# Performance work log

Hardware: AMD Instinct MI355X
Metric: run time of the kernel (lower is better)

Reference implementation:

```python
import jax, jax.numpy as jnp
import numpy as np

L, LM, B, D, H, DFF = 1024, 1024, 2, 512, 8, 2048
N = 16              # mamba d_state
DI = 2 * D          # mamba d_inner (expand=2)
DCONV = 4
DTR = (D + 15) // 16  # dt_rank = 32
EPS = 1e-5


def _rmsnorm(x, w):
    return x * w / jnp.sqrt(jnp.mean(x * x, -1, keepdims=True) + EPS)


def _layernorm(x, w, b):
    m = jnp.mean(x, -1, keepdims=True)
    v = jnp.mean((x - m) ** 2, -1, keepdims=True)
    return (x - m) / jnp.sqrt(v + EPS) * w + b


def _mha(q, k, v, in_w, in_b, out_w, out_b):
    # q: [Lq,B,D]; k,v: [Lk,B,D]
    Lq, Bb, Dd = q.shape
    Lk = k.shape[0]
    dh = Dd // H
    qp = (q @ in_w[:Dd].T + in_b[:Dd]).reshape(Lq, Bb, H, dh).transpose(1, 2, 0, 3)
    kp = (k @ in_w[Dd:2 * Dd].T + in_b[Dd:2 * Dd]).reshape(Lk, Bb, H, dh).transpose(1, 2, 0, 3)
    vp = (v @ in_w[2 * Dd:].T + in_b[2 * Dd:]).reshape(Lk, Bb, H, dh).transpose(1, 2, 0, 3)
    s = jnp.einsum('bhqd,bhkd->bhqk', qp, kp) * (dh ** -0.5)
    a = jax.nn.softmax(s, axis=-1)
    o = jnp.einsum('bhqk,bhkd->bhqd', a, vp).transpose(2, 0, 1, 3).reshape(Lq, Bb, Dd)
    return o @ out_w.T + out_b, jnp.mean(a, axis=1)  # attn averaged over heads


def _mamba(x, in_w, in_b, conv_w, conv_b, xproj_w, dt_w, dt_b, Alog, Dp, out_w, out_b):
    # x: [B,L,D] -> [B,L,D] selective state-space scan (mamba.py MambaBlock)
    xz = x @ in_w.T + in_b
    xm, z = xz[..., :DI], xz[..., DI:]
    # causal depthwise conv over time (pad left d_conv-1, truncate to L)
    xc = jax.lax.conv_general_dilated(
        xm.transpose(0, 2, 1), conv_w[:, None, :], (1,), [(DCONV - 1, 0)],
        feature_group_count=DI, dimension_numbers=('NCH', 'OIH', 'NCH'))
    xm = jax.nn.silu((xc + conv_b[None, :, None]).transpose(0, 2, 1))  # [B,L,DI]
    dbc = xm @ xproj_w.T
    dt, Bs, Cs = dbc[..., :DTR], dbc[..., DTR:DTR + N], dbc[..., DTR + N:]
    delta = jax.nn.softplus(dt @ dt_w.T + dt_b)           # [B,L,DI]
    A = -jnp.exp(Alog)                                    # [DI,N]
    dA = jnp.exp(delta[..., None] * A)                    # [B,L,DI,N]
    dBx = delta[..., None] * Bs[:, :, None, :] * xm[..., None]

    def step(h, ab):
        a, b = ab
        h = a * h + b
        return h, h

    _, hs = jax.lax.scan(step, jnp.zeros((x.shape[0], DI, N), x.dtype),
                         (dA.transpose(1, 0, 2, 3), dBx.transpose(1, 0, 2, 3)))
    y = jnp.einsum('blin,bln->bli', hs.transpose(1, 0, 2, 3), Cs)
    y = (y + Dp * xm) * jax.nn.silu(z)
    return y @ out_w.T + out_b


def _bimamba(x, ln1_w, ln1_b, ln2_w, ln2_b, f1_w, f1_b, f2_w, f2_b, mp):
    xn = _layernorm(x, ln1_w, ln1_b)
    mf = _mamba(xn, *mp)
    mb = jnp.flip(_mamba(jnp.flip(xn, 1), *mp), 1)
    m = _layernorm(mf + mb, ln2_w, ln2_b)
    ff = jax.nn.gelu(m @ f1_w.T + f1_b, approximate=False) @ f2_w.T + f2_b
    return ff + x


def _forward(tgt, memory,
             sa_in_w, sa_in_b, sa_out_w, sa_out_b,
             ca_in_w, ca_in_b, ca_out_w, ca_out_b,
             n1_w, n2_w, n3_w, n4_w,
             lin1_w, lin1_b, lin2_w, lin2_b,
             ln1_w, ln1_b, ln2_w, ln2_b,
             bff1_w, bff1_b, bff2_w, bff2_b,
             m_in_w, m_in_b, m_conv_w, m_conv_b, m_xproj_w,
             m_dt_w, m_dt_b, m_Alog, m_D, m_out_w, m_out_b):
    t2, _ = _mha(tgt, tgt, tgt, sa_in_w, sa_in_b, sa_out_w, sa_out_b)
    tgt = _rmsnorm(tgt + t2, n1_w)
    t2, attn = _mha(tgt, memory, memory, ca_in_w, ca_in_b, ca_out_w, ca_out_b)
    tgt = _rmsnorm(tgt + t2, n2_w)
    x = tgt.transpose(1, 0, 2)  # l b d -> b l d
    mp = (m_in_w, m_in_b, m_conv_w, m_conv_b, m_xproj_w, m_dt_w, m_dt_b, m_Alog, m_D, m_out_w, m_out_b)
    x = x + _bimamba(x, ln1_w, ln1_b, ln2_w, ln2_b, bff1_w, bff1_b, bff2_w, bff2_b, mp)
    tgt = x.transpose(1, 0, 2)
    tgt = _rmsnorm(tgt, n3_w)
    t2 = jax.nn.relu(tgt @ lin1_w.T + lin1_b) @ lin2_w.T + lin2_b
    tgt = _rmsnorm(tgt + t2, n4_w)
    return tgt, attn


def setup_inputs() -> dict:
    key = jax.random.key(0)
    ks = jax.random.split(key, 24)
    g = lambda i, shape, s=0.02: jax.random.normal(ks[i], shape, dtype=jnp.float32) * s
    inp = {
        'tgt': jax.random.normal(ks[0], (L, B, D), dtype=jnp.float32),
        'memory': jax.random.normal(ks[1], (LM, B, D), dtype=jnp.float32),
        'sa_in_w': g(2, (3 * D, D)), 'sa_in_b': jnp.zeros((3 * D,)),
        'sa_out_w': g(3, (D, D)), 'sa_out_b': jnp.zeros((D,)),
        'ca_in_w': g(4, (3 * D, D)), 'ca_in_b': jnp.zeros((3 * D,)),
        'ca_out_w': g(5, (D, D)), 'ca_out_b': jnp.zeros((D,)),
        'n1_w': jnp.ones((D,)), 'n2_w': jnp.ones((D,)),
        'n3_w': jnp.ones((D,)), 'n4_w': jnp.ones((D,)),
        'lin1_w': g(6, (DFF, D)), 'lin1_b': jnp.zeros((DFF,)),
        'lin2_w': g(7, (D, DFF)), 'lin2_b': jnp.zeros((D,)),
        'ln1_w': jnp.ones((D,)), 'ln1_b': jnp.zeros((D,)),
        'ln2_w': jnp.ones((D,)), 'ln2_b': jnp.zeros((D,)),
        'bff1_w': g(8, (4 * D, D)), 'bff1_b': jnp.zeros((4 * D,)),
        'bff2_w': g(9, (D, 4 * D)), 'bff2_b': jnp.zeros((D,)),
        'm_in_w': g(10, (2 * DI, D)), 'm_in_b': jnp.zeros((2 * DI,)),
        'm_conv_w': g(11, (DI, DCONV), 0.1), 'm_conv_b': jnp.zeros((DI,)),
        'm_xproj_w': g(12, (DTR + 2 * N, DI)),
        'm_dt_w': g(13, (DI, DTR), 0.1), 'm_dt_b': g(14, (DI,), 0.01),
        'm_Alog': jnp.log(jnp.tile(jnp.arange(1, N + 1, dtype=jnp.float32), (DI, 1))),
        'm_D': jnp.ones((DI,)),
        'm_out_w': g(15, (D, DI)), 'm_out_b': jnp.zeros((D,)),
    }
    return inp


def reference(tgt, memory,
              sa_in_w, sa_in_b, sa_out_w, sa_out_b,
              ca_in_w, ca_in_b, ca_out_w, ca_out_b,
              n1_w, n2_w, n3_w, n4_w,
              lin1_w, lin1_b, lin2_w, lin2_b,
              ln1_w, ln1_b, ln2_w, ln2_b,
              bff1_w, bff1_b, bff2_w, bff2_b,
              m_in_w, m_in_b, m_conv_w, m_conv_b, m_xproj_w,
              m_dt_w, m_dt_b, m_Alog, m_D, m_out_w, m_out_b):
    return _forward(tgt, memory,
                    sa_in_w, sa_in_b, sa_out_w, sa_out_b,
                    ca_in_w, ca_in_b, ca_out_w, ca_out_b,
                    n1_w, n2_w, n3_w, n4_w,
                    lin1_w, lin1_b, lin2_w, lin2_b,
                    ln1_w, ln1_b, ln2_w, ln2_b,
                    bff1_w, bff1_b, bff2_w, bff2_b,
                    m_in_w, m_in_b, m_conv_w, m_conv_b, m_xproj_w,
                    m_dt_w, m_dt_b, m_Alog, m_D, m_out_w, m_out_b)
```

## Files before the change

kernel.cpp:

```cpp
#include <hip/hip_runtime.h>
#include <hip/hip_bf16.h>
#include <math.h>

#define L_SEQ 1024
#define BB 2
#define DD 512
#define HH 8
#define DFFN 2048
#define NSTATE 16
#define DI 1024
#define EPSF 1e-5f

typedef __hip_bfloat16 bf16;
typedef __attribute__((ext_vector_type(8))) short short8v;
typedef __attribute__((ext_vector_type(4))) short short4v;
typedef __attribute__((ext_vector_type(4))) float float4v;

__device__ __forceinline__ float bf2f(bf16 v){ return __bfloat162float(v); }
__device__ __forceinline__ bf16 f2bf(float v){ return __float2bfloat16(v); }
__device__ __forceinline__ short f2bfs(float v){
  bf16 t = __float2bfloat16(v);
  short s; __builtin_memcpy(&s, &t, 2);
  return s;
}

__global__ void k_detect(const unsigned int* __restrict__ w, int* __restrict__ flag){
  __shared__ int cnt;
  if (threadIdx.x==0) cnt = 0;
  __syncthreads();
  unsigned int x = w[threadIdx.x];
  unsigned int low = x & 0xffffu;
  int e = (int)((low >> 7) & 0xffu);
  int vote = (low==0u) || (e >= 110 && e <= 140);
  atomicAdd(&cnt, vote);
  __syncthreads();
  if (threadIdx.x==0) flag[0] = (cnt >= 128) ? 1 : 0;
}

struct CvtTabF { const void* src[25]; unsigned int off[26]; };
struct CvtTabW { const void* src[12]; unsigned int off[13]; };

__global__ __launch_bounds__(256) void k_cvt_f32(CvtTabF t, float* __restrict__ dst,
                                                 const int* __restrict__ flag, int total){
  const int isbf = flag[0];
  for (int g = blockIdx.x*256 + threadIdx.x; g < total; g += gridDim.x*256){
    int k = 0;
    while (t.off[k+1] <= (unsigned int)g) ++k;
    int e = g - (int)t.off[k];
    dst[g] = isbf ? bf2f(((const bf16*)t.src[k])[e]) : ((const float*)t.src[k])[e];
  }
}

__global__ __launch_bounds__(256) void k_cvt_b16(CvtTabW t, bf16* __restrict__ dst,
                                                 const int* __restrict__ flag, int total){
  const int isbf = flag[0];
  for (int g = blockIdx.x*256 + threadIdx.x; g < total; g += gridDim.x*256){
    int k = 0;
    while (t.off[k+1] <= (unsigned int)g) ++k;
    int e = g - (int)t.off[k];
    if (isbf) dst[g] = ((const bf16*)t.src[k])[e];
    else      dst[g] = f2bf(((const float*)t.src[k])[e]);
  }
}

__global__ __launch_bounds__(256) void k_mfma_gemm(
    const void* __restrict__ Ab, int cA, long long sAb, long long sAh, long long sAm,
    const void* __restrict__ Bb, long long sBb, long long sBh, long long sBrow, int cB,
    void* __restrict__ Cb, int outBf, long long sCb, long long sCh, long long sCm,
    const float* __restrict__ bias, float scale, int act, int K, int H)
{
  __shared__ short As[64*40];
  __shared__ short Bs[64*40];
  const int tid = threadIdx.x;
  int bx = blockIdx.x, by = blockIdx.y;
  if (gridDim.z == 1 && (gridDim.y & 7) == 0){
    int gx = gridDim.x;
    int lin = by*gx + bx;
    int xcd = lin & 7, i = lin >> 3;
    by = xcd*(gridDim.y >> 3) + i / gx;
    bx = i % gx;
  }
  const int z = blockIdx.z; const int zb = z / H; const int zh = z % H;
  const int col0 = bx << 6, m0 = by << 6;
  const float* Af = (const float*)Ab;
  const bf16*  Aw = (const bf16*)Ab;
  const long long aoff = zb*sAb + zh*sAh;
  const float* Bf = (const float*)Bb;
  const bf16* Bw = (const bf16*)Bb;
  const long long boff = zb*sBb + zh*sBh;
  float4v acc[4];
  #pragma unroll
  for (int i=0;i<4;++i) acc[i] = (float4v)(0.f);
  const int lane = tid & 63, w = tid >> 6;
  const int lr = lane & 15, quad = lane >> 4;

  for (int k0 = 0; k0 < K; k0 += 32){
    if (cA == 1){
      int row = tid >> 2, k8 = (tid & 3) << 3;
      short8v v = *(const short8v*)&Aw[aoff + (long long)(m0+row)*sAm + k0 + k8];
      *(short8v*)&As[row*40 + k8] = v;
    } else {
      #pragma unroll
      for (int i=0;i<2;++i){
        int g = tid + i*256;
        int row = g >> 3, k4 = (g & 7) << 2;
        float4 v = *(const float4*)&Af[aoff + (long long)(m0+row)*sAm + k0 + k4];
        short4v s4; s4.x=f2bfs(v.x); s4.y=f2bfs(v.y); s4.z=f2bfs(v.z); s4.w=f2bfs(v.w);
        *(short4v*)&As[row*40 + k4] = s4;
      }
    }
    if (cB == 2){
      int row = tid >> 2, k8 = (tid & 3) << 3;
      short8v v = *(const short8v*)&Bw[boff + (long long)(col0+row)*sBrow + k0 + k8];
      *(short8v*)&Bs[row*40 + k8] = v;
    } else {
      #pragma unroll
      for (int i=0;i<2;++i){
        int g = tid + i*256;
        int row = g >> 3, k4 = (g & 7) << 2;
        float4 v = *(const float4*)&Bf[boff + (long long)(col0+row)*sBrow + k0 + k4];
        short4v s4; s4.x=f2bfs(v.x); s4.y=f2bfs(v.y); s4.z=f2bfs(v.z); s4.w=f2bfs(v.w);
        *(short4v*)&Bs[row*40 + k4] = s4;
      }
    }
    __syncthreads();
    short8v a = *(short8v*)&As[(w*16 + lr)*40 + quad*8];
    #pragma unroll
    for (int cb=0; cb<4; ++cb){
      short8v bfr = *(short8v*)&Bs[(cb*16 + lr)*40 + quad*8];
      acc[cb] = __builtin_amdgcn_mfma_f32_16x16x32_bf16(a, bfr, acc[cb], 0, 0, 0);
    }
    __syncthreads();
  }
  #pragma unroll
  for (int cb=0; cb<4; ++cb){
    #pragma unroll
    for (int r=0;r<4;++r){
      int m = m0 + w*16 + quad*4 + r;
      int n = col0 + cb*16 + lr;
      float v = acc[cb][r] * scale;
      if (bias) v += bias[n];
      if (act==1) v = fmaxf(v,0.f);
      else if (act==2) v = 0.5f*v*(1.f + erff(v*0.70710678118654752f));
      else if (act==3) v = fmaxf(v,0.f) + log1pf(__expf(-fabsf(v)));
      if (outBf) ((bf16*)Cb)[zb*sCb + zh*sCh + (long long)m*sCm + n] = f2bf(v);
      else       ((float*)Cb)[zb*sCb + zh*sCh + (long long)m*sCm + n] = v;
    }
  }
}

__global__ __launch_bounds__(256) void k_gemm_sk(
    const void* __restrict__ Ab, int cA, long long sAz, long long sAm,
    const bf16* __restrict__ Bw, long long sBrow,
    float* __restrict__ Cb, long long sCz, long long sCm,
    const float* __restrict__ bias, int K, int KS)
{
  __shared__ short As[64*40];
  __shared__ short Bs[64*40];
  const int tid = threadIdx.x;
  int bx, by, bz;
  {
    int gx = gridDim.x, gy = gridDim.y, gz = gridDim.z;
    int lin = ((int)blockIdx.z*gy + blockIdx.y)*gx + blockIdx.x;
    int xcd = lin & 7, i = lin >> 3;
    bx = i % gx; int rest = i / gx;
    int pair = xcd * ((gy*gz) >> 3) + rest;
    by = pair % gy; bz = pair / gy;
  }
  const int zb = bz / KS, kc = bz % KS;
  const int Kc = K / KS;
  const int col0 = bx << 6, m0 = by << 6;
  const float* Af = (const float*)Ab;
  const bf16*  Aw = (const bf16*)Ab;
  const long long aoff = (long long)zb*sAz;
  float4v acc[4];
  #pragma unroll
  for (int i=0;i<4;++i) acc[i] = (float4v)(0.f);
  const int lane = tid & 63, w = tid >> 6;
  const int lr = lane & 15, quad = lane >> 4;

  const int kbeg = kc*Kc;
  for (int k0 = kbeg; k0 < kbeg + Kc; k0 += 32){
    if (cA == 1){
      int row = tid >> 2, k8 = (tid & 3) << 3;
      *(short8v*)&As[row*40 + k8] =
        *(const short8v*)&Aw[aoff + (long long)(m0+row)*sAm + k0 + k8];
    } else {
      #pragma unroll
      for (int i=0;i<2;++i){
        int g = tid + i*256;
        int row = g >> 3, k4 = (g & 7) << 2;
        float4 v = *(const float4*)&Af[aoff + (long long)(m0+row)*sAm + k0 + k4];
        short4v s4; s4.x=f2bfs(v.x); s4.y=f2bfs(v.y); s4.z=f2bfs(v.z); s4.w=f2bfs(v.w);
        *(short4v*)&As[row*40 + k4] = s4;
      }
    }
    {
      int row = tid >> 2, k8 = (tid & 3) << 3;
      *(short8v*)&Bs[row*40 + k8] =
        *(const short8v*)&Bw[(long long)(col0+row)*sBrow + k0 + k8];
    }
    __syncthreads();
    short8v a = *(short8v*)&As[(w*16 + lr)*40 + quad*8];
    #pragma unroll
    for (int cb=0; cb<4; ++cb){
      short8v bfr = *(short8v*)&Bs[(cb*16 + lr)*40 + quad*8];
      acc[cb] = __builtin_amdgcn_mfma_f32_16x16x32_bf16(a, bfr, acc[cb], 0, 0, 0);
    }
    __syncthreads();
  }
  #pragma unroll
  for (int cb=0; cb<4; ++cb){
    #pragma unroll
    for (int r=0;r<4;++r){
      int m = m0 + w*16 + quad*4 + r;
      int n = col0 + cb*16 + lr;
      float v = acc[cb][r];
      if (kc == 0 && bias) v += bias[n];
      atomicAdd(&Cb[(long long)zb*sCz + (long long)m*sCm + n], v);
    }
  }
}

__global__ __launch_bounds__(256) void k_flash2(
    const bf16* __restrict__ Qb, int ldq, int qoff,
    const bf16* __restrict__ Kb, int ldk, int koff,
    const bf16* __restrict__ Vb, int ldv, int voff,
    float* __restrict__ Opart, float* __restrict__ Ml, float scale)
{
  __shared__ short Qs[64*40];
  __shared__ short Ks[64*40];
  __shared__ short Vs[64*40];
  __shared__ short Ps[64*40];
  const int tid = threadIdx.x;
  const int q0 = blockIdx.x << 6;
  const int z = blockIdx.y; const int b = z >> 3; const int hoff = (z & 7) << 6;
  const int kc = blockIdx.z;
  const int lane = tid & 63, w = tid >> 6;
  const int lr = lane & 15, quad = lane >> 4;

  #pragma unroll
  for (int i=0;i<2;++i){
    int idx = tid + i*256;
    int row = idx >> 3, d8 = (idx & 7) << 3;
    *(short8v*)&Qs[row*40 + d8] =
      *(const short8v*)&Qb[(size_t)((q0+row)*BB + b)*ldq + qoff + hoff + d8];
  }

  float m_r[4], l_r[4];
  #pragma unroll
  for (int r=0;r<4;++r){ m_r[r] = -1e30f; l_r[r] = 0.f; }
  float4v acc_o[4];
  #pragma unroll
  for (int cb=0;cb<4;++cb) acc_o[cb] = (float4v)(0.f);

  short8v kr[2], vr[2];
  #pragma unroll
  for (int i=0;i<2;++i){
    int idx = tid + i*256;
    int row = kc*256 + (idx >> 3); int d8 = (idx & 7) << 3;
    kr[i] = *(const short8v*)&Kb[(size_t)(row*BB + b)*ldk + koff + hoff + d8];
    vr[i] = *(const short8v*)&Vb[(size_t)(row*BB + b)*ldv + voff + hoff + d8];
  }

  for (int kt=0; kt<4; ++kt){
    __syncthreads();
    #pragma unroll
    for (int i=0;i<2;++i){
      int idx = tid + i*256;
      int row = idx >> 3, d8 = (idx & 7) << 3;
      *(short8v*)&Ks[row*40 + d8] = kr[i];
      int sc = row ^ d8;
      #pragma unroll
      for (int j=0;j<8;++j) Vs[(d8+j)*40 + sc] = vr[i][j];
    }
    if (kt < 3){
      #pragma unroll
      for (int i=0;i<2;++i){
        int idx = tid + i*256;
        int row = kc*256 + (kt+1)*64 + (idx >> 3); int d8 = (idx & 7) << 3;
        kr[i] = *(const short8v*)&Kb[(size_t)(row*BB + b)*ldk + koff + hoff + d8];
        vr[i] = *(const short8v*)&Vb[(size_t)(row*BB + b)*ldv + voff + hoff + d8];
      }
    }
    __syncthreads();
    short8v a0 = *(short8v*)&Qs[(w*16+lr)*40 + quad*8];
    short8v a1 = *(short8v*)&Qs[(w*16+lr)*40 + quad*8 + 32];
    float4v s[4];
    #pragma unroll
    for (int cb=0;cb<4;++cb){
      short8v b0 = *(short8v*)&Ks[(cb*16+lr)*40 + quad*8];
      short8v b1 = *(short8v*)&Ks[(cb*16+lr)*40 + quad*8 + 32];
      float4v t = __builtin_amdgcn_mfma_f32_16x16x32_bf16(a0, b0, (float4v)(0.f), 0,0,0);
      s[cb] = __builtin_amdgcn_mfma_f32_16x16x32_bf16(a1, b1, t, 0,0,0);
    }
    #pragma unroll
    for (int cb=0;cb<4;++cb)
      #pragma unroll
      for (int r=0;r<4;++r) s[cb][r] *= scale;
    float al[4];
    #pragma unroll
    for (int r=0;r<4;++r){
      float mx = fmaxf(fmaxf(s[0][r],s[1][r]),fmaxf(s[2][r],s[3][r]));
      #pragma unroll
      for (int ofs=1; ofs<16; ofs<<=1) mx = fmaxf(mx, __shfl_xor(mx, ofs));
      float mnew = fmaxf(m_r[r], mx);
      al[r] = __expf(m_r[r] - mnew);
      float sum = 0.f;
      #pragma unroll
      for (int cb=0;cb<4;++cb){
        float p = __expf(s[cb][r] - mnew);
        s[cb][r] = p;
        sum += p;
      }
      #pragma unroll
      for (int ofs=1; ofs<16; ofs<<=1) sum += __shfl_xor(sum, ofs);
      l_r[r] = l_r[r]*al[r] + sum;
      m_r[r] = mnew;
    }
    #pragma unroll
    for (int cb=0;cb<4;++cb)
      #pragma unroll
      for (int r=0;r<4;++r){
        acc_o[cb][r] *= al[r];
        Ps[(w*16 + quad*4 + r)*40 + cb*16 + lr] = f2bfs(s[cb][r]);
      }
    __syncthreads();
    short8v p0 = *(short8v*)&Ps[(w*16+lr)*40 + quad*8];
    short8v p1 = *(short8v*)&Ps[(w*16+lr)*40 + quad*8 + 32];
    #pragma unroll
    for (int cb=0;cb<4;++cb){
      int dcol = cb*16 + lr;
      int sw = (dcol >> 3) & 7;
      short8v v0 = *(short8v*)&Vs[dcol*40 + ((quad ^ sw) << 3)];
      short8v v1 = *(short8v*)&Vs[dcol*40 + (((quad+4) ^ sw) << 3)];
      acc_o[cb] = __builtin_amdgcn_mfma_f32_16x16x32_bf16(p0, v0, acc_o[cb], 0,0,0);
      acc_o[cb] = __builtin_amdgcn_mfma_f32_16x16x32_bf16(p1, v1, acc_o[cb], 0,0,0);
    }
  }
  #pragma unroll
  for (int r=0;r<4;++r){
    int row = q0 + w*16 + quad*4 + r;
    size_t obase = ((size_t)(kc*16 + z)*1024 + row)*64;
    #pragma unroll
    for (int cb=0;cb<4;++cb)
      Opart[obase + cb*16 + lr] = acc_o[cb][r];
    if (lr == 0){
      size_t mi = ((size_t)kc*16384 + z*1024 + row)*2;
      Ml[mi] = m_r[r]; Ml[mi+1] = l_r[r];
    }
  }
}

__global__ __launch_bounds__(256) void k_fcomb(const float* __restrict__ Opart, const float* __restrict__ Ml,
                                               bf16* __restrict__ O, float* __restrict__ Mfin)
{
  int gid = blockIdx.x*256 + threadIdx.x;
  int row = gid >> 6, d = gid & 63;
  int z = row >> 10, q = row & 1023;
  float m[4], l[4];
  #pragma unroll
  for (int kc=0;kc<4;++kc){
    size_t mi = ((size_t)kc*16384 + row)*2;
    m[kc] = Ml[mi]; l[kc] = Ml[mi+1];
  }
  float ms = fmaxf(fmaxf(m[0],m[1]),fmaxf(m[2],m[3]));
  float c[4]; float ls = 0.f;
  #pragma unroll
  for (int kc=0;kc<4;++kc){ c[kc] = __expf(m[kc]-ms); ls += l[kc]*c[kc]; }
  float o = 0.f;
  #pragma unroll
  for (int kc=0;kc<4;++kc) o += Opart[((size_t)kc*16384 + row)*64 + d] * c[kc];
  o /= ls;
  int b = z >> 3, hoff = (z & 7) << 6;
  O[((size_t)q*BB + b)*512 + hoff + d] = f2bf(o);
  if (d == 0){ Mfin[(size_t)row*2] = ms; Mfin[(size_t)row*2+1] = ls; }
}

__global__ __launch_bounds__(256) void k_pmean(
    const bf16* __restrict__ Qb, int ldq,
    const bf16* __restrict__ Kb, int ldk,
    const float* __restrict__ Mfin, void* __restrict__ out,
    const int* __restrict__ flag, float scale)
{
  __shared__ short Qs[64*40];
  __shared__ short Ks[64*40];
  const int tid = threadIdx.x;
  const int k0 = blockIdx.x << 6, q0 = blockIdx.y << 6;
  const int b = blockIdx.z;
  const int lane = tid & 63, w = tid >> 6;
  const int lr = lane & 15, quad = lane >> 4;
  float acc[4][4];
  #pragma unroll
  for (int cb=0;cb<4;++cb)
    #pragma unroll
    for (int r=0;r<4;++r) acc[cb][r] = 0.f;

  for (int h=0; h<8; ++h){
    int z = b*8 + h, hoff = h << 6;
    __syncthreads();
    #pragma unroll
    for (int i=0;i<2;++i){
      int idx = tid + i*256;
      int row = idx >> 3, d8 = (idx & 7) << 3;
      *(short8v*)&Qs[row*40 + d8] = *(const short8v*)&Qb[((size_t)(q0+row)*BB + b)*ldq + hoff + d8];
      *(short8v*)&Ks[row*40 + d8] = *(const short8v*)&Kb[((size_t)(k0+row)*BB + b)*ldk + hoff + d8];
    }
    __syncthreads();
    float mm[4], li[4];
    #pragma unroll
    for (int r=0;r<4;++r){
      int qrow = q0 + w*16 + quad*4 + r;
      size_t mi = ((size_t)z*1024 + qrow)*2;
      mm[r] = Mfin[mi]; li[r] = 1.f/Mfin[mi+1];
    }
    short8v a0 = *(short8v*)&Qs[(w*16+lr)*40 + quad*8];
    short8v a1 = *(short8v*)&Qs[(w*16+lr)*40 + quad*8 + 32];
    #pragma unroll
    for (int cb=0;cb<4;++cb){
      short8v b0 = *(short8v*)&Ks[(cb*16+lr)*40 + quad*8];
      short8v b1 = *(short8v*)&Ks[(cb*16+lr)*40 + quad*8 + 32];
      float4v t = __builtin_amdgcn_mfma_f32_16x16x32_bf16(a0, b0, (float4v)(0.f), 0,0,0);
      t = __builtin_amdgcn_mfma_f32_16x16x32_bf16(a1, b1, t, 0,0,0);
      #pragma unroll
      for (int r=0;r<4;++r)
        acc[cb][r] += __expf(t[r]*scale - mm[r]) * li[r];
    }
  }
  #pragma unroll
  for (int cb=0;cb<4;++cb)
    #pragma unroll
    for (int r=0;r<4;++r){
      int q = q0 + w*16 + quad*4 + r;
      int k = k0 + cb*16 + lr;
      float v = acc[cb][r] * 0.125f;
      size_t o = (size_t)(1u<<20) + ((size_t)b<<20) + (size_t)q*1024 + k;
      if (flag[0]) ((bf16*)out)[o] = f2bf(v);
      else         ((float*)out)[o] = v;
    }
}

__global__ __launch_bounds__(256) void k_add_rmsnorm(float* __restrict__ x, const float* __restrict__ t2, const float* __restrict__ w){
  int row = blockIdx.x; size_t base = (size_t)row*DD;
  int tid = threadIdx.x;
  float v0 = x[base+tid] + t2[base+tid];
  float v1 = x[base+tid+256] + t2[base+tid+256];
  __shared__ float red[256];
  red[tid] = v0*v0 + v1*v1; __syncthreads();
  for (int s=128;s>0;s>>=1){ if(tid<s) red[tid]+=red[tid+s]; __syncthreads(); }
  float rms = rsqrtf(red[0]*(1.f/DD) + EPSF);
  x[base+tid]     = v0 * w[tid]     * rms;
  x[base+tid+256] = v1 * w[tid+256] * rms;
}

__global__ __launch_bounds__(256) void k_add_rmsnorm_out(const float* __restrict__ x, const float* __restrict__ t2,
                                                         const float* __restrict__ w, void* __restrict__ out,
                                                         const int* __restrict__ flag){
  int row = blockIdx.x; size_t base = (size_t)row*DD;
  int tid = threadIdx.x;
  float v0 = x[base+tid] + t2[base+tid];
  float v1 = x[base+tid+256] + t2[base+tid+256];
  __shared__ float red[256];
  red[tid] = v0*v0 + v1*v1; __syncthreads();
  for (int s=128;s>0;s>>=1){ if(tid<s) red[tid]+=red[tid+s]; __syncthreads(); }
  float rms = rsqrtf(red[0]*(1.f/DD) + EPSF);
  float o0 = v0 * w[tid]     * rms;
  float o1 = v1 * w[tid+256] * rms;
  if (flag[0]){ ((bf16*)out)[base+tid] = f2bf(o0); ((bf16*)out)[base+tid+256] = f2bf(o1); }
  else        { ((float*)out)[base+tid] = o0;      ((float*)out)[base+tid+256] = o1; }
}

__global__ __launch_bounds__(256) void k_trans_layernorm(const float* __restrict__ tgt, const float* __restrict__ w, const float* __restrict__ bias, bf16* __restrict__ xn){
  int r = blockIdx.x;
  int b = r >> 10, l = r & 1023;
  size_t src = ((size_t)l*BB + b)*DD;
  int tid = threadIdx.x;
  float v0 = tgt[src+tid], v1 = tgt[src+tid+256];
  __shared__ float red[256];
  red[tid] = v0 + v1; __syncthreads();
  for (int s=128;s>0;s>>=1){ if(tid<s) red[tid]+=red[tid+s]; __syncthreads(); }
  float mean = red[0]*(1.f/DD);
  __syncthreads();
  red[tid] = v0*v0 + v1*v1; __syncthreads();
  for (int s=128;s>0;s>>=1){ if(tid<s) red[tid]+=red[tid+s]; __syncthreads(); }
  float var = red[0]*(1.f/DD) - mean*mean;
  float rstd = rsqrtf(var + EPSF);
  size_t dst = (size_t)r*DD;
  xn[dst+tid]     = f2bf((v0-mean)*rstd*w[tid]     + bias[tid]);
  xn[dst+tid+256] = f2bf((v1-mean)*rstd*w[tid+256] + bias[tid+256]);
}

__global__ __launch_bounds__(256) void k_combine_ln(const float* __restrict__ yf, const float* __restrict__ yb, const float* __restrict__ w, const float* __restrict__ bias, bf16* __restrict__ mo){
  int r = blockIdx.x; int b = r>>10, l = r&1023;
  size_t rf = (size_t)r*DD;
  size_t rb = ((size_t)(b<<10) + (1023 - l))*DD;
  int tid = threadIdx.x;
  float v0 = yf[rf+tid]     + yb[rb+tid];
  float v1 = yf[rf+tid+256] + yb[rb+tid+256];
  __shared__ float red[256];
  red[tid] = v0 + v1; __syncthreads();
  for (int s=128;s>0;s>>=1){ if(tid<s) red[tid]+=red[tid+s]; __syncthreads(); }
  float mean = red[0]*(1.f/DD);
  __syncthreads();
  red[tid] = v0*v0 + v1*v1; __syncthreads();
  for (int s=128;s>0;s>>=1){ if(tid<s) red[tid]+=red[tid+s]; __syncthreads(); }
  float var = red[0]*(1.f/DD) - mean*mean;
  float rstd = rsqrtf(var + EPSF);
  mo[rf+tid]     = f2bf((v0-mean)*rstd*w[tid]     + bias[tid]);
  mo[rf+tid+256] = f2bf((v1-mean)*rstd*w[tid+256] + bias[tid+256]);
}

__global__ __launch_bounds__(256) void k_bimamba_final(float* __restrict__ tgt, const float* __restrict__ ffo, const float* __restrict__ w){
  int r = blockIdx.x; int b = r>>10, l = r&1023;
  size_t t = ((size_t)l*BB + b)*DD;
  size_t f = (size_t)r*DD;
  int tid = threadIdx.x;
  float v0 = 2.f*tgt[t+tid]     + ffo[f+tid];
  float v1 = 2.f*tgt[t+tid+256] + ffo[f+tid+256];
  __shared__ float red[256];
  red[tid] = v0*v0 + v1*v1; __syncthreads();
  for (int s=128;s>0;s>>=1){ if(tid<s) red[tid]+=red[tid+s]; __syncthreads(); }
  float rms = rsqrtf(red[0]*(1.f/DD) + EPSF);
  tgt[t+tid]     = v0 * w[tid]     * rms;
  tgt[t+tid+256] = v1 * w[tid+256] * rms;
}

__global__ __launch_bounds__(256) void k_conv_silu(const float* __restrict__ xz, const float* __restrict__ cw, const float* __restrict__ cb, float* __restrict__ xmc){
  int rev = blockIdx.y;
  int idx = blockIdx.x*256 + threadIdx.x;
  int c = idx & 1023;
  int l = (idx >> 10) & 1023;
  int b = idx >> 20;
  float acc = cb[c];
  float w4[4];
  #pragma unroll
  for (int j=0;j<4;++j) w4[j] = cw[(c<<2)+j];
  #pragma unroll
  for (int j=0;j<4;++j){
    int t = l - 3 + j;
    if (t >= 0){
      int src = rev ? (1023 - t) : t;
      acc = fmaf(w4[j], xz[((size_t)(b<<10) + src)*2048 + c], acc);
    }
  }
  xmc[(size_t)rev*(2u<<20) + idx] = acc / (1.f + __expf(-acc));
}

__global__ __launch_bounds__(256) void k_scan1(
    const float* __restrict__ delta_f, const float* __restrict__ delta_b,
    const float* __restrict__ xmc_f,  const float* __restrict__ xmc_b,
    const float* __restrict__ dbc_f,  const float* __restrict__ dbc_b,
    const float* __restrict__ Alog,
    float* __restrict__ hend, float* __restrict__ Sdl)
{
  int ch = blockIdx.x*256 + threadIdx.x;
  int c = blockIdx.y;
  int dir = ch >> 11, b = (ch >> 10) & 1, d = ch & 1023;
  const float* delta = dir ? delta_b : delta_f;
  const float* xmc   = dir ? xmc_b   : xmc_f;
  const float* dbc   = dir ? dbc_b   : dbc_f;
  float Av[NSTATE];
  #pragma unroll
  for (int n=0;n<NSTATE;++n) Av[n] = -__expf(Alog[d*NSTATE+n]);
  float h[NSTATE];
  #pragma unroll
  for (int n=0;n<NSTATE;++n) h[n]=0.f;
  float S = 0.f;
  int r0 = b*1024 + c*32;
  for (int t=0;t<32;++t){
    int r = r0 + t;
    float dl = delta[((size_t)r<<10) + d];
    float x  = xmc[((size_t)r<<10) + d];
    const float4* bp = (const float4*)(dbc + (size_t)r*64 + 32);
    float Bv[NSTATE];
    ((float4*)Bv)[0]=bp[0]; ((float4*)Bv)[1]=bp[1]; ((float4*)Bv)[2]=bp[2]; ((float4*)Bv)[3]=bp[3];
    S += dl;
    float dx = dl*x;
    #pragma unroll
    for (int n=0;n<NSTATE;++n){
      float dA = __expf(dl*Av[n]);
      h[n] = fmaf(dA, h[n], dx*Bv[n]);
    }
  }
  size_t base = ((size_t)c*4096 + ch)*16;
  #pragma unroll
  for (int n=0;n<NSTATE;++n) hend[base+n] = h[n];
  Sdl[c*4096 + ch] = S;
}

__global__ __launch_bounds__(256) void k_scan_carry(const float* __restrict__ Alog,
                                                    float* __restrict__ hh, const float* __restrict__ Sdl)
{
  int g = blockIdx.x*256 + threadIdx.x;
  int ch = g >> 4, n = g & 15;
  int d = ch & 1023;
  float Av = -__expf(Alog[d*16+n]);
  float h = 0.f;
  for (int c=0;c<32;++c){
    size_t base = ((size_t)c*4096 + ch)*16 + n;
    float he = hh[base];
    hh[base] = h;
    h = fmaf(__expf(Av*Sdl[c*4096+ch]), h, he);
  }
}

__global__ __launch_bounds__(256) void k_scan2(
    const float* __restrict__ delta_f, const float* __restrict__ delta_b,
    const float* __restrict__ xmc_f,  const float* __restrict__ xmc_b,
    const float* __restrict__ dbc_f,  const float* __restrict__ dbc_b,
    const float* __restrict__ Alog,   const float* __restrict__ hin,
    const float* __restrict__ xz,     const float* __restrict__ Dp,
    bf16* __restrict__ yo)
{
  int ch = blockIdx.x*256 + threadIdx.x;
  int c = blockIdx.y;
  int dir = ch >> 11, b = (ch >> 10) & 1, d = ch & 1023;
  const float* delta = dir ? delta_b : delta_f;
  const float* xmc   = dir ? xmc_b   : xmc_f;
  const float* dbc   = dir ? dbc_b   : dbc_f;
  float Av[NSTATE];
  #pragma unroll
  for (int n=0;n<NSTATE;++n) Av[n] = -__expf(Alog[d*NSTATE+n]);
  float h[NSTATE];
  size_t cbase = ((size_t)c*4096 + ch)*16;
  #pragma unroll
  for (int n=0;n<NSTATE;++n) h[n] = hin[cbase+n];
  float Dd = Dp[d];
  int r0 = b*1024 + c*32;
  for (int t=0;t<32;++t){
    int r = r0 + t;
    int lidx = c*32 + t;
    float dl = delta[((size_t)r<<10) + d];
    float x  = xmc[((size_t)r<<10) + d];
    const float4* bp = (const float4*)(dbc + (size_t)r*64 + 32);
    float Bv[NSTATE], Cv[NSTATE];
    ((float4*)Bv)[0]=bp[0]; ((float4*)Bv)[1]=bp[1]; ((float4*)Bv)[2]=bp[2]; ((float4*)Bv)[3]=bp[3];
    ((float4*)Cv)[0]=bp[4]; ((float4*)Cv)[1]=bp[5]; ((float4*)Cv)[2]=bp[6]; ((float4*)Cv)[3]=bp[7];
    float dx = dl*x;
    float acc = 0.f;
    #pragma unroll
    for (int n=0;n<NSTATE;++n){
      float dA = __expf(dl*Av[n]);
      h[n] = fmaf(dA, h[n], dx*Bv[n]);
      acc = fmaf(h[n], Cv[n], acc);
    }
    int src = dir ? (1023 - lidx) : lidx;
    float zz = xz[((size_t)(b<<10) + src)*2048 + 1024 + d];
    float sg = zz / (1.f + __expf(-zz));
    yo[(size_t)dir*(2u<<20) + ((size_t)r<<10) + d] = f2bf((acc + Dd*x) * sg);
  }
}

extern "C" void kernel_launch(void* const* d_in, const int* in_sizes, int n_in,
                              void* d_out, int out_size, void* d_ws, size_t ws_size,
                              hipStream_t stream)
{
  if (n_in < 37) return;
  static const unsigned int SZ[37] = {
    1048576,1048576,786432,1536,262144,512,786432,1536,262144,512,
    512,512,512,512,1048576,2048,1048576,512,512,512,
    512,512,1048576,2048,1048576,512,1048576,2048,4096,1024,
    65536,32768,1024,16384,1024,524288,512
  };
  static const unsigned char ISW[37] = {
    0,0,1,0,1,0,1,0,1,0, 0,0,0,0,1,0,1,0,0,0,
    0,0,1,0,1,0,1,0,0,0, 1,1,0,0,0,1,0
  };
  const long long MF = 1u<<20;
  if (ws_size < (size_t)(32*MF)*sizeof(float)) return;

  float* ws = (float*)d_ws;
  float* inF = ws;
  bf16*  inB = (bf16*)(ws + 3*MF);
  float* t2    = ws + 7*MF;
  float* mbuf  = ws + 8*MF;
  float* proj  = ws + 9*MF;
  float* big   = ws + 12*MF;
  float* ff1   = ws + 28*MF;
  float* hend  = ws + 30*MF;

  CvtTabF tf; CvtTabW tb;
  unsigned int fOff[37], bOff[37];
  {
    int nf=0, nb=0; unsigned int of=0, ob=0;
    for (int i=0;i<37;++i){
      if (ISW[i]){ tb.src[nb]=d_in[i]; tb.off[nb]=ob; bOff[i]=ob; ob+=SZ[i]; ++nb; }
      else       { tf.src[nf]=d_in[i]; tf.off[nf]=of; fOff[i]=of; of+=SZ[i]; ++nf; }
    }
    tf.off[25]=of; tb.off[12]=ob;
    int* flag = (int*)(ws + 3*MF - 16);

    #define PF(i) (inF + fOff[i])
    #define PW(i) (inB + bOff[i])

    float* tgt_f = PF(0);
    float* mem_f = PF(1);
    bf16* qkvB   = (bf16*)proj;
    bf16* qB     = (bf16*)proj;
    bf16* kvB    = (bf16*)(proj + 1*MF);
    bf16* attnoB = (bf16*)mbuf;
    bf16* xnB    = (bf16*)t2;
    float* Opart   = big;
    float* Ml      = big + 4*MF;
    float* Mfin    = big + 4*MF + 131072;
    float* xz      = big;
    float* xmc_f   = big + 4*MF;
    float* xmc_b   = xmc_f + 2*MF;
    float* delta_f = big + 8*MF;
    float* delta_b = big + 10*MF;
    float* dbc_f   = proj;
    float* dbc_b   = proj + 131072;
    float* Sdl     = proj + 262144;
    float* yproj_f = proj + 1*MF;
    float* yproj_b = proj + 2*MF;
    float* ffo     = mem_f;
    bf16*  ybf     = (bf16*)ff1;
    bf16*  ff1B    = (bf16*)ff1;
    bf16*  mbufB   = (bf16*)mbuf;

    k_detect<<<1,256,0,stream>>>((const unsigned int*)d_in[0], flag);
    k_cvt_f32<<<2048,256,0,stream>>>(tf, inF, flag, (int)of);
    k_cvt_b16<<<4096,256,0,stream>>>(tb, inB, flag, (int)ob);

    k_mfma_gemm<<<dim3(24,32,1),256,0,stream>>>(tgt_f,0,0,0,512, PW(2),0,0,512,2, qkvB,1,0,0,1536, PF(3),1.f,0,512,1);
    k_flash2<<<dim3(16,16,4),256,0,stream>>>(qkvB,1536,0, qkvB,1536,512, qkvB,1536,1024, Opart, Ml, 0.125f);
    k_fcomb<<<4096,256,0,stream>>>(Opart, Ml, attnoB, Mfin);
    hipMemsetAsync(t2, 0, (size_t)MF*4, stream);
    k_gemm_sk<<<dim3(8,32,2),256,0,stream>>>(attnoB,1,0,512, PW(4),512, t2,0,512, PF(5), 512, 2);
    k_add_rmsnorm<<<2048,256,0,stream>>>(tgt_f, t2, PF(10));

    k_mfma_gemm<<<dim3(8,32,1),256,0,stream>>>(tgt_f,0,0,0,512, PW(6),0,0,512,2, qB,1,0,0,512, PF(7),1.f,0,512,1);
    k_mfma_gemm<<<dim3(16,32,1),256,0,stream>>>(mem_f,0,0,0,512, PW(6)+(size_t)512*512,0,0,512,2, kvB,1,0,0,1024, PF(7)+512,1.f,0,512,1);
    k_flash2<<<dim3(16,16,4),256,0,stream>>>(qB,512,0, kvB,1024,0, kvB,1024,512, Opart, Ml, 0.125f);
    k_fcomb<<<4096,256,0,stream>>>(Opart, Ml, attnoB, Mfin);
    k_pmean<<<dim3(16,16,2),256,0,stream>>>(qB,512, kvB,1024, Mfin, d_out, flag, 0.125f);
    hipMemsetAsync(t2, 0, (size_t)MF*4, stream);
    k_gemm_sk<<<dim3(8,32,2),256,0,stream>>>(attnoB,1,0,512, PW(8),512, t2,0,512, PF(9), 512, 2);
    k_add_rmsnorm<<<2048,256,0,stream>>>(tgt_f, t2, PF(11));

    k_trans_layernorm<<<2048,256,0,stream>>>(tgt_f, PF(18), PF(19), xnB);
    k_mfma_gemm<<<dim3(32,32,1),256,0,stream>>>(xnB,1,0,0,512, PW(26),0,0,512,2, xz,0,0,0,2048, PF(27),1.f,0,512,1);
    k_conv_silu<<<dim3(8192,2),256,0,stream>>>(xz, PF(28), PF(29), xmc_f);
    hipMemsetAsync(dbc_f, 0, (size_t)262144*4, stream);
    k_gemm_sk<<<dim3(1,32,8),256,0,stream>>>(xmc_f,0,2*MF,1024, PW(30),1024, dbc_f,131072,64, nullptr, 1024, 4);
    k_mfma_gemm<<<dim3(16,32,2),256,0,stream>>>(dbc_f,0,131072,0,64, PW(31),0,0,32,2, delta_f,0,2*MF,0,1024, PF(32),1.f,3,32,1);
    k_scan1<<<dim3(16,32),256,0,stream>>>(delta_f,delta_b,xmc_f,xmc_b,dbc_f,dbc_b, PF(33), hend, Sdl);
    k_scan_carry<<<256,256,0,stream>>>(PF(33), hend, Sdl);
    k_scan2<<<dim3(16,32),256,0,stream>>>(delta_f,delta_b,xmc_f,xmc_b,dbc_f,dbc_b, PF(33), hend, xz, PF(34), ybf);
    hipMemsetAsync(yproj_f, 0, (size_t)2*MF*4, stream);
    k_gemm_sk<<<dim3(8,32,4),256,0,stream>>>(ybf,1,2*MF,1024, PW(35),1024, yproj_f,1*MF,512, PF(36), 1024, 2);
    k_combine_ln<<<2048,256,0,stream>>>(yproj_f, yproj_b, PF(20), PF(21), mbufB);
    k_mfma_gemm<<<dim3(32,32,1),256,0,stream>>>(mbufB,1,0,0,512, PW(22),0,0,512,2, ff1B,1,0,0,2048, PF(23),1.f,2,512,1);
    hipMemsetAsync(ffo, 0, (size_t)MF*4, stream);
    k_gemm_sk<<<dim3(8,32,4),256,0,stream>>>(ff1B,1,0,2048, PW(24),2048, ffo,0,512, PF(25), 2048, 4);
    k_bimamba_final<<<2048,256,0,stream>>>(tgt_f, ffo, PF(12));

    k_mfma_gemm<<<dim3(32,32,1),256,0,stream>>>(tgt_f,0,0,0,512, PW(14),0,0,512,2, ff1B,1,0,0,2048, PF(15),1.f,1,512,1);
    hipMemsetAsync(t2, 0, (size_t)MF*4, stream);
    k_gemm_sk<<<dim3(8,32,4),256,0,stream>>>(ff1B,1,0,2048, PW(16),2048, t2,0,512, PF(17), 2048, 4);
    k_add_rmsnorm_out<<<2048,256,0,stream>>>(tgt_f, t2, PF(13), d_out, flag);
    #undef PF
    #undef PW
  }
}
```

Measured before the change: 625.7 us.

## Split flash and scan into more chunks, store mamba intermediates in bf16, use power-table decay

Flash attention now splits the key range into 8 chunks instead of 4, and the combine kernel merges 8 partial results. The selective scan uses 64 time chunks of 16 instead of 32 of 32, and the scratch buffers are moved to make room for this. The conv/silu output and delta are stored as bf16 to halve their memory traffic. When A matches -(n+1), which holds for the test initialisation, the 16 decay exponentials are replaced by powers of a single exp(-delta). A runtime check falls back to the exact path otherwise, and the bf16 storage lowers precision.

```diff
diff --git a/kernel.cpp b/kernel.cpp
--- a/kernel.cpp
+++ b/kernel.cpp
@@ -22,6 +22,14 @@
   bf16 t = __float2bfloat16(v);
   short s; __builtin_memcpy(&s, &t, 2);
   return s;
+}
+
+__device__ __forceinline__ void powtab(float q1, float* dA){
+  float q2=q1*q1, q4=q2*q2, q8=q4*q4;
+  dA[0]=q1;       dA[1]=q2;       dA[2]=q2*q1;     dA[3]=q4;
+  dA[4]=q4*q1;    dA[5]=q4*q2;    dA[6]=q4*q2*q1;  dA[7]=q8;
+  dA[8]=q8*q1;    dA[9]=q8*q2;    dA[10]=q8*q2*q1; dA[11]=q8*q4;
+  dA[12]=q8*q4*q1;dA[13]=q8*q4*q2;dA[14]=q8*q4*q2*q1;dA[15]=q8*q8;
 }
 
 __global__ void k_detect(const unsigned int* __restrict__ w, int* __restrict__ flag){
@@ -258,12 +266,12 @@
   #pragma unroll
   for (int i=0;i<2;++i){
     int idx = tid + i*256;
-    int row = kc*256 + (idx >> 3); int d8 = (idx & 7) << 3;
+    int row = kc*128 + (idx >> 3); int d8 = (idx & 7) << 3;
     kr[i] = *(const short8v*)&Kb[(size_t)(row*BB + b)*ldk + koff + hoff + d8];
     vr[i] = *(const short8v*)&Vb[(size_t)(row*BB + b)*ldv + voff + hoff + d8];
   }
 
-  for (int kt=0; kt<4; ++kt){
+  for (int kt=0; kt<2; ++kt){
     __syncthreads();
     #pragma unroll
     for (int i=0;i<2;++i){
@@ -274,11 +282,11 @@
       #pragma unroll
       for (int j=0;j<8;++j) Vs[(d8+j)*40 + sc] = vr[i][j];
     }
-    if (kt < 3){
+    if (kt < 1){
       #pragma unroll
       for (int i=0;i<2;++i){
         int idx = tid + i*256;
-        int row = kc*256 + (kt+1)*64 + (idx >> 3); int d8 = (idx & 7) << 3;
+        int row = kc*128 + 64 + (idx >> 3); int d8 = (idx & 7) << 3;
         kr[i] = *(const short8v*)&Kb[(size_t)(row*BB + b)*ldk + koff + hoff + d8];
         vr[i] = *(const short8v*)&Vb[(size_t)(row*BB + b)*ldv + voff + hoff + d8];
       }
@@ -358,19 +366,22 @@
   int gid = blockIdx.x*256 + threadIdx.x;
   int row = gid >> 6, d = gid & 63;
   int z = row >> 10, q = row & 1023;
-  float m[4], l[4];
-  #pragma unroll
-  for (int kc=0;kc<4;++kc){
+  float m[8], l[8];
+  #pragma unroll
+  for (int kc=0;kc<8;++kc){
     size_t mi = ((size_t)kc*16384 + row)*2;
     m[kc] = Ml[mi]; l[kc] = Ml[mi+1];
   }
-  float ms = fmaxf(fmaxf(m[0],m[1]),fmaxf(m[2],m[3]));
-  float c[4]; float ls = 0.f;
-  #pragma unroll
-  for (int kc=0;kc<4;++kc){ c[kc] = __expf(m[kc]-ms); ls += l[kc]*c[kc]; }
-  float o = 0.f;
-  #pragma unroll
-  for (int kc=0;kc<4;++kc) o += Opart[((size_t)kc*16384 + row)*64 + d] * c[kc];
+  float ms = -1e30f;
+  #pragma unroll
+  for (int kc=0;kc<8;++kc) ms = fmaxf(ms, m[kc]);
+  float ls = 0.f, o = 0.f;
+  #pragma unroll
+  for (int kc=0;kc<8;++kc){
+    float c = __expf(m[kc]-ms);
+    ls += l[kc]*c;
+    o  += Opart[((size_t)kc*16384 + row)*64 + d] * c;
+  }
   o /= ls;
   int b = z >> 3, hoff = (z & 7) << 6;
   O[((size_t)q*BB + b)*512 + hoff + d] = f2bf(o);
@@ -525,7 +536,7 @@
   tgt[t+tid+256] = v1 * w[tid+256] * rms;
 }
 
-__global__ __launch_bounds__(256) void k_conv_silu(const float* __restrict__ xz, const float* __restrict__ cw, const float* __restrict__ cb, float* __restrict__ xmc){
+__global__ __launch_bounds__(256) void k_conv_silu(const float* __restrict__ xz, const float* __restrict__ cw, const float* __restrict__ cb, bf16* __restrict__ xmc){
   int rev = blockIdx.y;
   int idx = blockIdx.x*256 + threadIdx.x;
   int c = idx & 1023;
@@ -543,12 +554,12 @@
       acc = fmaf(w4[j], xz[((size_t)(b<<10) + src)*2048 + c], acc);
     }
   }
-  xmc[(size_t)rev*(2u<<20) + idx] = acc / (1.f + __expf(-acc));
+  xmc[(size_t)rev*(2u<<20) + idx] = f2bf(acc / (1.f + __expf(-acc)));
 }
 
 __global__ __launch_bounds__(256) void k_scan1(
-    const float* __restrict__ delta_f, const float* __restrict__ delta_b,
-    const float* __restrict__ xmc_f,  const float* __restrict__ xmc_b,
+    const bf16* __restrict__ delta_f, const bf16* __restrict__ delta_b,
+    const bf16* __restrict__ xmc_f,  const bf16* __restrict__ xmc_b,
     const float* __restrict__ dbc_f,  const float* __restrict__ dbc_b,
     const float* __restrict__ Alog,
     float* __restrict__ hend, float* __restrict__ Sdl)
@@ -556,31 +567,38 @@
   int ch = blockIdx.x*256 + threadIdx.x;
   int c = blockIdx.y;
   int dir = ch >> 11, b = (ch >> 10) & 1, d = ch & 1023;
-  const float* delta = dir ? delta_b : delta_f;
-  const float* xmc   = dir ? xmc_b   : xmc_f;
-  const float* dbc   = dir ? dbc_b   : dbc_f;
-  float Av[NSTATE];
-  #pragma unroll
-  for (int n=0;n<NSTATE;++n) Av[n] = -__expf(Alog[d*NSTATE+n]);
+  const bf16* delta = dir ? delta_b : delta_f;
+  const bf16* xmc   = dir ? xmc_b   : xmc_f;
+  const float* dbc  = dir ? dbc_b   : dbc_f;
+  float Av[NSTATE]; bool fast = true;
+  #pragma unroll
+  for (int n=0;n<NSTATE;++n){
+    Av[n] = -__expf(Alog[d*NSTATE+n]);
+    fast = fast && (fabsf(Av[n] + (float)(n+1)) < 1e-4f*(float)(n+1));
+  }
   float h[NSTATE];
   #pragma unroll
   for (int n=0;n<NSTATE;++n) h[n]=0.f;
   float S = 0.f;
-  int r0 = b*1024 + c*32;
-  for (int t=0;t<32;++t){
+  int r0 = b*1024 + c*16;
+  for (int t=0;t<16;++t){
     int r = r0 + t;
-    float dl = delta[((size_t)r<<10) + d];
-    float x  = xmc[((size_t)r<<10) + d];
+    float dl = bf2f(delta[((size_t)r<<10) + d]);
+    float x  = bf2f(xmc[((size_t)r<<10) + d]);
     const float4* bp = (const float4*)(dbc + (size_t)r*64 + 32);
     float Bv[NSTATE];
     ((float4*)Bv)[0]=bp[0]; ((float4*)Bv)[1]=bp[1]; ((float4*)Bv)[2]=bp[2]; ((float4*)Bv)[3]=bp[3];
     S += dl;
     float dx = dl*x;
-    #pragma unroll
-    for (int n=0;n<NSTATE;++n){
-      float dA = __expf(dl*Av[n]);
-      h[n] = fmaf(dA, h[n], dx*Bv[n]);
-    }
+    float dA[NSTATE];
+    if (fast){ powtab(__expf(-dl), dA); }
+    else {
+      #pragma unroll
+      for (int n=0;n<NSTATE;++n) dA[n] = __expf(dl*Av[n]);
+    }
+    #pragma unroll
+    for (int n=0;n<NSTATE;++n)
+      h[n] = fmaf(dA[n], h[n], dx*Bv[n]);
   }
   size_t base = ((size_t)c*4096 + ch)*16;
   #pragma unroll
@@ -596,7 +614,7 @@
   int d = ch & 1023;
   float Av = -__expf(Alog[d*16+n]);
   float h = 0.f;
-  for (int c=0;c<32;++c){
+  for (int c=0;c<64;++c){
     size_t base = ((size_t)c*4096 + ch)*16 + n;
     float he = hh[base];
     hh[base] = h;
@@ -605,8 +623,8 @@
 }
 
 __global__ __launch_bounds__(256) void k_scan2(
-    const float* __restrict__ delta_f, const float* __restrict__ delta_b,
-    const float* __restrict__ xmc_f,  const float* __restrict__ xmc_b,
+    const bf16* __restrict__ delta_f, const bf16* __restrict__ delta_b,
+    const bf16* __restrict__ xmc_f,  const bf16* __restrict__ xmc_b,
     const float* __restrict__ dbc_f,  const float* __restrict__ dbc_b,
     const float* __restrict__ Alog,   const float* __restrict__ hin,
     const float* __restrict__ xz,     const float* __restrict__ Dp,
@@ -615,35 +633,46 @@
   int ch = blockIdx.x*256 + threadIdx.x;
   int c = blockIdx.y;
   int dir = ch >> 11, b = (ch >> 10) & 1, d = ch & 1023;
-  const float* delta = dir ? delta_b : delta_f;
-  const float* xmc   = dir ? xmc_b   : xmc_f;
-  const float* dbc   = dir ? dbc_b   : dbc_f;
-  float Av[NSTATE];
-  #pragma unroll
-  for (int n=0;n<NSTATE;++n) Av[n] = -__expf(Alog[d*NSTATE+n]);
+  const bf16* delta = dir ? delta_b : delta_f;
+  const bf16* xmc   = dir ? xmc_b   : xmc_f;
+  const float* dbc  = dir ? dbc_b   : dbc_f;
+  float Av[NSTATE]; bool fast = true;
+  #pragma unroll
+  for (int n=0;n<NSTATE;++n){
+    Av[n] = -__expf(Alog[d*NSTATE+n]);
+    fast = fast && (fabsf(Av[n] + (float)(n+1)) < 1e-4f*(float)(n+1));
+  }
   float h[NSTATE];
   size_t cbase = ((size_t)c*4096 + ch)*16;
   #pragma unroll
   for (int n=0;n<NSTATE;++n) h[n] = hin[cbase+n];
   float Dd = Dp[d];
-  int r0 = b*1024 + c*32;
-  for (int t=0;t<32;++t){
+  int r0 = b*1024 + c*16;
+  for (int t=0;t<16;++t){
     int r = r0 + t;
-    int lidx = c*32 + t;
-    float dl = delta[((size_t)r<<10) + d];
-    float x  = xmc[((size_t)r<<10) + d];
+    int lidx = c*16 + t;
+    float dl = bf2f(delta[((size_t)r<<10) + d]);
+    float x  = bf2f(xmc[((size_t)r<<10) + d]);
     const float4* bp = (const float4*)(dbc + (size_t)r*64 + 32);
     float Bv[NSTATE], Cv[NSTATE];
     ((float4*)Bv)[0]=bp[0]; ((float4*)Bv)[1]=bp[1]; ((float4*)Bv)[2]=bp[2]; ((float4*)Bv)[3]=bp[3];
     ((float4*)Cv)[0]=bp[4]; ((float4*)Cv)[1]=bp[5]; ((float4*)Cv)[2]=bp[6]; ((float4*)Cv)[3]=bp[7];
     float dx = dl*x;
-    float acc = 0.f;
-    #pragma unroll
-    for (int n=0;n<NSTATE;++n){
-      float dA = __expf(dl*Av[n]);
-      h[n] = fmaf(dA, h[n], dx*Bv[n]);
-      acc = fmaf(h[n], Cv[n], acc);
-    }
+    float dA[NSTATE];
+    if (fast){ powtab(__expf(-dl), dA); }
+    else {
+      #pragma unroll
+      for (int n=0;n<NSTATE;++n) dA[n] = __expf(dl*Av[n]);
+    }
+    float acc0 = 0.f, acc1 = 0.f;
+    #pragma unroll
+    for (int n=0;n<NSTATE;n+=2){
+      h[n]   = fmaf(dA[n],   h[n],   dx*Bv[n]);
+      h[n+1] = fmaf(dA[n+1], h[n+1], dx*Bv[n+1]);
+      acc0 = fmaf(h[n],   Cv[n],   acc0);
+      acc1 = fmaf(h[n+1], Cv[n+1], acc1);
+    }
+    float acc = acc0 + acc1;
     int src = dir ? (1023 - lidx) : lidx;
     float zz = xz[((size_t)(b<<10) + src)*2048 + 1024 + d];
     float sg = zz / (1.f + __expf(-zz));
@@ -677,7 +706,6 @@
   float* proj  = ws + 9*MF;
   float* big   = ws + 12*MF;
   float* ff1   = ws + 28*MF;
-  float* hend  = ws + 30*MF;
 
   CvtTabF tf; CvtTabW tb;
   unsigned int fOff[37], bOff[37];
@@ -701,16 +729,17 @@
     bf16* attnoB = (bf16*)mbuf;
     bf16* xnB    = (bf16*)t2;
     float* Opart   = big;
-    float* Ml      = big + 4*MF;
-    float* Mfin    = big + 4*MF + 131072;
+    float* Ml      = big + 8*MF;
+    float* Mfin    = big + 8*MF + 262144;
     float* xz      = big;
-    float* xmc_f   = big + 4*MF;
-    float* xmc_b   = xmc_f + 2*MF;
-    float* delta_f = big + 8*MF;
-    float* delta_b = big + 10*MF;
+    bf16*  xmc_f   = (bf16*)(big + 4*MF);
+    bf16*  xmc_b   = (bf16*)(big + 5*MF);
+    bf16*  delta_f = (bf16*)(big + 6*MF);
+    bf16*  delta_b = (bf16*)(big + 7*MF);
+    float* hend    = big + 8*MF;
+    float* Sdl     = big + 12*MF;
     float* dbc_f   = proj;
     float* dbc_b   = proj + 131072;
-    float* Sdl     = proj + 262144;
     float* yproj_f = proj + 1*MF;
     float* yproj_b = proj + 2*MF;
     float* ffo     = mem_f;
@@ -723,7 +752,7 @@
     k_cvt_b16<<<4096,256,0,stream>>>(tb, inB, flag, (int)ob);
 
     k_mfma_gemm<<<dim3(24,32,1),256,0,stream>>>(tgt_f,0,0,0,512, PW(2),0,0,512,2, qkvB,1,0,0,1536, PF(3),1.f,0,512,1);
-    k_flash2<<<dim3(16,16,4),256,0,stream>>>(qkvB,1536,0, qkvB,1536,512, qkvB,1536,1024, Opart, Ml, 0.125f);
+    k_flash2<<<dim3(16,16,8),256,0,stream>>>(qkvB,1536,0, qkvB,1536,512, qkvB,1536,1024, Opart, Ml, 0.125f);
     k_fcomb<<<4096,256,0,stream>>>(Opart, Ml, attnoB, Mfin);
     hipMemsetAsync(t2, 0, (size_t)MF*4, stream);
     k_gemm_sk<<<dim3(8,32,2),256,0,stream>>>(attnoB,1,0,512, PW(4),512, t2,0,512, PF(5), 512, 2);
@@ -731,7 +760,7 @@
 
     k_mfma_gemm<<<dim3(8,32,1),256,0,stream>>>(tgt_f,0,0,0,512, PW(6),0,0,512,2, qB,1,0,0,512, PF(7),1.f,0,512,1);
     k_mfma_gemm<<<dim3(16,32,1),256,0,stream>>>(mem_f,0,0,0,512, PW(6)+(size_t)512*512,0,0,512,2, kvB,1,0,0,1024, PF(7)+512,1.f,0,512,1);
-    k_flash2<<<dim3(16,16,4),256,0,stream>>>(qB,512,0, kvB,1024,0, kvB,1024,512, Opart, Ml, 0.125f);
+    k_flash2<<<dim3(16,16,8),256,0,stream>>>(qB,512,0, kvB,1024,0, kvB,1024,512, Opart, Ml, 0.125f);
     k_fcomb<<<4096,256,0,stream>>>(Opart, Ml, attnoB, Mfin);
     k_pmean<<<dim3(16,16,2),256,0,stream>>>(qB,512, kvB,1024, Mfin, d_out, flag, 0.125f);
     hipMemsetAsync(t2, 0, (size_t)MF*4, stream);
@@ -742,11 +771,11 @@
     k_mfma_gemm<<<dim3(32,32,1),256,0,stream>>>(xnB,1,0,0,512, PW(26),0,0,512,2, xz,0,0,0,2048, PF(27),1.f,0,512,1);
     k_conv_silu<<<dim3(8192,2),256,0,stream>>>(xz, PF(28), PF(29), xmc_f);
     hipMemsetAsync(dbc_f, 0, (size_t)262144*4, stream);
-    k_gemm_sk<<<dim3(1,32,8),256,0,stream>>>(xmc_f,0,2*MF,1024, PW(30),1024, dbc_f,131072,64, nullptr, 1024, 4);
-    k_mfma_gemm<<<dim3(16,32,2),256,0,stream>>>(dbc_f,0,131072,0,64, PW(31),0,0,32,2, delta_f,0,2*MF,0,1024, PF(32),1.f,3,32,1);
-    k_scan1<<<dim3(16,32),256,0,stream>>>(delta_f,delta_b,xmc_f,xmc_b,dbc_f,dbc_b, PF(33), hend, Sdl);
+    k_gemm_sk<<<dim3(1,32,8),256,0,stream>>>(xmc_f,1,2*MF,1024, PW(30),1024, dbc_f,131072,64, nullptr, 1024, 4);
+    k_mfma_gemm<<<dim3(16,32,2),256,0,stream>>>(dbc_f,0,131072,0,64, PW(31),0,0,32,2, delta_f,1,2*MF,0,1024, PF(32),1.f,3,32,1);
+    k_scan1<<<dim3(16,64),256,0,stream>>>(delta_f,delta_b,xmc_f,xmc_b,dbc_f,dbc_b, PF(33), hend, Sdl);
     k_scan_carry<<<256,256,0,stream>>>(PF(33), hend, Sdl);
-    k_scan2<<<dim3(16,32),256,0,stream>>>(delta_f,delta_b,xmc_f,xmc_b,dbc_f,dbc_b, PF(33), hend, xz, PF(34), ybf);
+    k_scan2<<<dim3(16,64),256,0,stream>>>(delta_f,delta_b,xmc_f,xmc_b,dbc_f,dbc_b, PF(33), hend, xz, PF(34), ybf);
     hipMemsetAsync(yproj_f, 0, (size_t)2*MF*4, stream);
     k_gemm_sk<<<dim3(8,32,4),256,0,stream>>>(ybf,1,2*MF,1024, PW(35),1024, yproj_f,1*MF,512, PF(36), 1024, 2);
     k_combine_ln<<<2048,256,0,stream>>>(yproj_f, yproj_b, PF(20), PF(21), mbufB);
```

Measured after the change: 612.5 us. 1.02x faster.
